# Kernel tuning notes

Hardware: AMD Instinct MI355X
Metric: run time of the kernel (lower is better)

The kernel has to match this reference:

```python
import jax, jax.numpy as jnp
import numpy as np

N_NODES = 30000
N_EDGES = 480000
NEG_SLOPE = 0.2  # PyG GATConv default negative_slope


def setup_inputs() -> dict:
    key = jax.random.key(0)
    ks = jax.random.split(key, 10)

    def glorot(k, shape, fan):
        return jax.random.normal(k, shape, jnp.float32) * (1.0 / np.sqrt(fan))

    x = jax.random.normal(ks[0], (N_NODES, 1024), jnp.float32)
    edge_index = jax.random.randint(ks[1], (2, N_EDGES), 0, N_NODES)
    # layer 1: in=1024 -> heads=8, C=64, concat -> 512
    W1 = glorot(ks[2], (1024, 512), 1024)
    a1_src = glorot(ks[3], (8, 64), 64)
    a1_dst = glorot(ks[4], (8, 64), 64)
    b1 = jnp.zeros((512,), jnp.float32)
    # layer 2: in=512 -> heads=1, C=256, no concat
    W2 = glorot(ks[5], (512, 256), 512)
    a2_src = glorot(ks[6], (1, 256), 256)
    a2_dst = glorot(ks[7], (1, 256), 256)
    b2 = jnp.zeros((256,), jnp.float32)
    return {"x": x, "edge_index": edge_index, "W1": W1, "a1_src": a1_src,
            "a1_dst": a1_dst, "b1": b1, "W2": W2, "a2_src": a2_src,
            "a2_dst": a2_dst, "b2": b2}


def gat_conv(x, src, dst, W, a_src, a_dst, bias, heads, channels, concat):
    """PyG-style GATConv (self-loops already included in src/dst)."""
    n = x.shape[0]
    h = (x @ W).reshape(n, heads, channels)          # [N, H, C]
    al_s = jnp.einsum('nhc,hc->nh', h, a_src)        # per-node src logits
    al_d = jnp.einsum('nhc,hc->nh', h, a_dst)        # per-node dst logits
    e = jax.nn.leaky_relu(al_s[src] + al_d[dst], NEG_SLOPE)   # [E, H]
    # segment softmax over edges grouped by destination node
    m = jax.ops.segment_max(e, dst, num_segments=n)
    p = jnp.exp(e - m[dst])
    s = jax.ops.segment_sum(p, dst, num_segments=n)
    alpha = p / s[dst]                               # [E, H]
    out = jax.ops.segment_sum(alpha[:, :, None] * h[src], dst, num_segments=n)
    out = out.reshape(n, heads * channels) if concat else out.mean(axis=1)
    return out + bias


def reference(x, edge_index, W1, a1_src, a1_dst, b1, W2, a2_src, a2_dst, b2):
    n = x.shape[0]
    loops = jnp.arange(n, dtype=edge_index.dtype)
    src = jnp.concatenate([edge_index[0], loops])    # add self-loops (PyG default)
    dst = jnp.concatenate([edge_index[1], loops])
    # eval mode: dropout is identity
    h = jax.nn.elu(gat_conv(x, src, dst, W1, a1_src, a1_dst, b1, 8, 64, True))
    out = gat_conv(h, src, dst, W2, a2_src, a2_dst, b2, 1, 256, False)
    return out
```

## Files before the change

### kernel.cpp

```cpp
#include <hip/hip_runtime.h>
#include <hip/hip_bf16.h>

typedef unsigned int uint;
typedef unsigned short ushort;
typedef __attribute__((ext_vector_type(8))) short short8;
typedef __attribute__((ext_vector_type(4))) short short4v;
typedef __attribute__((ext_vector_type(4))) float f32x4;

#define LEAKY 0.2f

__device__ __forceinline__ ushort f2bf(float f) {
  __hip_bfloat16 h = __float2bfloat16(f);
  return __builtin_bit_cast(ushort, h);
}
__device__ __forceinline__ float bf2f(ushort u) {
  uint v = ((uint)u) << 16;
  return __builtin_bit_cast(float, v);
}
__device__ __forceinline__ void gload_lds16(const void* g, void* l) {
  __builtin_amdgcn_global_load_lds(
      (const __attribute__((address_space(1))) void*)g,
      (__attribute__((address_space(3))) void*)l, 16, 0, 0);
}

__global__ void convw(const float* __restrict__ W, ushort* __restrict__ Wt,
                      int K, int N) {
  int idx = blockIdx.x * 256 + threadIdx.x;
  if (idx >= K * N) return;
  int nrow = idx / K;
  int k = idx - nrow * K;
  Wt[idx] = f2bf(W[(size_t)k * N + nrow]);
}

__global__ void zero2(int* a, int* b, int n) {
  int i = blockIdx.x * 256 + threadIdx.x;
  if (i < n) { a[i] = 0; b[i] = 0; }
}

__global__ void hist(const int* __restrict__ dst, int E, int n, int* cnt) {
  int e = blockIdx.x * 256 + threadIdx.x;
  if (e >= E + n) return;
  int d = (e < E) ? dst[e] : (e - E);
  atomicAdd(&cnt[d], 1);
}

__global__ __launch_bounds__(1024) void scan_fast(const int* __restrict__ cnt,
                                                  int* __restrict__ rp, int n) {
  __shared__ int wsum[16];
  __shared__ int woff[16];
  const int t = threadIdx.x;
  const int per = (n + 1023) / 1024;
  const int base = t * per;
  int local[32];
  int s = 0;
#pragma unroll
  for (int i = 0; i < 32; i++) {
    if (i >= per) break;
    int idx = base + i;
    int v = (idx < n) ? cnt[idx] : 0;
    local[i] = s;
    s += v;
  }
  const int lane = t & 63, wave = t >> 6;
  int incl = s;
#pragma unroll
  for (int off = 1; off < 64; off <<= 1) {
    int v = __shfl_up(incl, off);
    if (lane >= off) incl += v;
  }
  if (lane == 63) wsum[wave] = incl;
  __syncthreads();
  if (wave == 0 && lane < 16) {
    int v = wsum[lane];
    int wi = v;
#pragma unroll
    for (int off = 1; off < 16; off <<= 1) {
      int u = __shfl_up(wi, off);
      if (lane >= off) wi += u;
    }
    woff[lane] = wi - v;
  }
  __syncthreads();
  const int gexcl = woff[wave] + (incl - s);
#pragma unroll
  for (int i = 0; i < 32; i++) {
    if (i >= per) break;
    int idx = base + i;
    if (idx < n) rp[idx] = gexcl + local[i];
  }
  if (t == 1023) rp[n] = woff[15] + incl;
}

__global__ void scatter(const int* __restrict__ src, const int* __restrict__ dst,
                        int E, int n, const int* __restrict__ rp,
                        int* fill, int* __restrict__ csr) {
  int e = blockIdx.x * 256 + threadIdx.x;
  if (e >= E + n) return;
  int s, d;
  if (e < E) { s = src[e]; d = dst[e]; } else { s = d = e - E; }
  int pos = rp[d] + atomicAdd(&fill[d], 1);
  csr[pos] = s;
}

template <int ABYTES>
__global__ __launch_bounds__(512) void gemm_wide(
    const void* __restrict__ Av, const ushort* __restrict__ Bt,
    ushort* __restrict__ C, int M, int K, int N) {
  constexpr int BM = 128, BN = 256, BK = 32;
  constexpr int SPRA = (BK * ABYTES) / 16;
  constexpr int A_ITER = (BM * SPRA) / 512;
  __shared__ __align__(16) char As[BM * BK * ABYTES];
  __shared__ __align__(16) char Bs[BN * BK * 2];
  const int tid = threadIdx.x;
  const int wave = tid >> 6, lane = tid & 63;
  const int g = lane >> 4, r16 = lane & 15;
  const int nby = N / BN;
  const int bx = (int)blockIdx.x / nby;
  const int by = (int)blockIdx.x - bx * nby;
  const int bm = bx * BM, bn = by * BN;
  const int wm = (wave >> 2) * 64, wn = (wave & 3) * 64;

  f32x4 acc[4][4] = {};
  const char* A = (const char*)Av;

  for (int k0 = 0; k0 < K; k0 += BK) {
#pragma unroll
    for (int i = 0; i < A_ITER; i++) {
      int slot = i * 512 + tid;
      int row = slot / SPRA;
      int cp = slot % SPRA;
      int key = (ABYTES == 4) ? (row & 7) : ((row >> 1) & 3);
      int cl = cp ^ key;
      int arow = bm + row;
      arow = arow < M ? arow : M - 1;
      const char* gp = A + ((size_t)arow * K + k0) * ABYTES + cl * 16;
      char* lp = As + (i * 512 + wave * 64) * 16;
      gload_lds16(gp, lp);
    }
#pragma unroll
    for (int i = 0; i < 2; i++) {
      int slot = i * 512 + tid;
      int row = slot >> 2;
      int cp = slot & 3;
      int cl = cp ^ ((row >> 1) & 3);
      const char* gp = (const char*)(Bt + (size_t)(bn + row) * K + k0 + cl * 8);
      char* lp = Bs + (i * 512 + wave * 64) * 16;
      gload_lds16(gp, lp);
    }
    asm volatile("s_waitcnt vmcnt(0)" ::: "memory");
    __syncthreads();

    short8 af[4], bfr[4];
#pragma unroll
    for (int mi = 0; mi < 4; mi++) {
      int row = wm + mi * 16 + r16;
      if constexpr (ABYTES == 4) {
        int key = row & 7;
        f32x4 lo = *(const f32x4*)(As + (row * 8 + ((2 * g) ^ key)) * 16);
        f32x4 hi = *(const f32x4*)(As + (row * 8 + ((2 * g + 1) ^ key)) * 16);
        short8 s;
#pragma unroll
        for (int q = 0; q < 4; q++) {
          s[q] = (short)f2bf(lo[q]);
          s[q + 4] = (short)f2bf(hi[q]);
        }
        af[mi] = s;
      } else {
        int key = (row >> 1) & 3;
        af[mi] = *(const short8*)(As + (row * 4 + (g ^ key)) * 16);
      }
    }
#pragma unroll
    for (int ni = 0; ni < 4; ni++) {
      int row = wn + ni * 16 + r16;
      int key = (row >> 1) & 3;
      bfr[ni] = *(const short8*)(Bs + (row * 4 + (g ^ key)) * 16);
    }
#pragma unroll
    for (int mi = 0; mi < 4; mi++)
#pragma unroll
      for (int ni = 0; ni < 4; ni++)
        acc[mi][ni] = __builtin_amdgcn_mfma_f32_16x16x32_bf16(
            af[mi], bfr[ni], acc[mi][ni], 0, 0, 0);
    __syncthreads();
  }

#pragma unroll
  for (int mi = 0; mi < 4; mi++) {
#pragma unroll
    for (int j = 0; j < 4; j++) {
      int row = bm + wm + mi * 16 + g * 4 + j;
      if (row < M) {
#pragma unroll
        for (int ni = 0; ni < 4; ni++) {
          int col = bn + wn + ni * 16 + r16;
          C[(size_t)row * N + col] = f2bf(acc[mi][ni][j]);
        }
      }
    }
  }
}

__global__ void logits1(const ushort* __restrict__ h1, const float* __restrict__ a_s,
                        const float* __restrict__ a_d, float* __restrict__ al_s,
                        float* __restrict__ al_d, int n) {
  int node = blockIdx.x * 4 + (threadIdx.x >> 6);
  if (node >= n) return;
  int lane = threadIdx.x & 63;
  int c0 = lane * 8;
  short8 hv = *(const short8*)&h1[(size_t)node * 512 + c0];
  float ps = 0.f, pd = 0.f;
#pragma unroll
  for (int j = 0; j < 8; j++) {
    float f = bf2f((ushort)hv[j]);
    ps += f * a_s[c0 + j];
    pd += f * a_d[c0 + j];
  }
#pragma unroll
  for (int m = 1; m < 8; m <<= 1) {
    ps += __shfl_xor(ps, m);
    pd += __shfl_xor(pd, m);
  }
  if ((lane & 7) == 0) {
    al_s[node * 8 + (lane >> 3)] = ps;
    al_d[node * 8 + (lane >> 3)] = pd;
  }
}

__global__ void logits2(const ushort* __restrict__ h2, const float* __restrict__ a_s,
                        const float* __restrict__ a_d, float* __restrict__ al_s,
                        float* __restrict__ al_d, int n) {
  int node = blockIdx.x * 4 + (threadIdx.x >> 6);
  if (node >= n) return;
  int lane = threadIdx.x & 63;
  int c0 = lane * 4;
  short4v hv = *(const short4v*)&h2[(size_t)node * 256 + c0];
  float ps = 0.f, pd = 0.f;
#pragma unroll
  for (int j = 0; j < 4; j++) {
    float f = bf2f((ushort)hv[j]);
    ps += f * a_s[c0 + j];
    pd += f * a_d[c0 + j];
  }
#pragma unroll
  for (int m = 1; m < 64; m <<= 1) {
    ps += __shfl_xor(ps, m);
    pd += __shfl_xor(pd, m);
  }
  if (lane == 0) {
    al_s[node] = ps;
    al_d[node] = pd;
  }
}

__global__ void agg1(const int* __restrict__ rp, const int* __restrict__ csr,
                     const ushort* __restrict__ h1, const float* __restrict__ al_s,
                     const float* __restrict__ al_d, const float* __restrict__ b1,
                     ushort* __restrict__ h2in, int n) {
  int node = blockIdx.x * 4 + (threadIdx.x >> 6);
  if (node >= n) return;
  int lane = threadIdx.x & 63;
  int head = lane >> 3, c0 = lane * 8;
  float ad = al_d[node * 8 + head];
  int beg = rp[node], end = rp[node + 1];
  float sum = 0.f;
  float acc[8] = {};
  int j = beg;
  for (; j + 4 <= end; j += 4) {
    int s0 = csr[j], s1 = csr[j + 1], s2 = csr[j + 2], s3 = csr[j + 3];
    float e0 = al_s[s0 * 8 + head] + ad;
    float e1 = al_s[s1 * 8 + head] + ad;
    float e2 = al_s[s2 * 8 + head] + ad;
    float e3 = al_s[s3 * 8 + head] + ad;
    short8 v0 = *(const short8*)&h1[(size_t)s0 * 512 + c0];
    short8 v1 = *(const short8*)&h1[(size_t)s1 * 512 + c0];
    short8 v2 = *(const short8*)&h1[(size_t)s2 * 512 + c0];
    short8 v3 = *(const short8*)&h1[(size_t)s3 * 512 + c0];
    e0 = e0 > 0.f ? e0 : LEAKY * e0;
    e1 = e1 > 0.f ? e1 : LEAKY * e1;
    e2 = e2 > 0.f ? e2 : LEAKY * e2;
    e3 = e3 > 0.f ? e3 : LEAKY * e3;
    float p0 = __expf(e0), p1 = __expf(e1), p2 = __expf(e2), p3 = __expf(e3);
    sum += (p0 + p1) + (p2 + p3);
#pragma unroll
    for (int q = 0; q < 8; q++)
      acc[q] += p0 * bf2f((ushort)v0[q]) + p1 * bf2f((ushort)v1[q]) +
                p2 * bf2f((ushort)v2[q]) + p3 * bf2f((ushort)v3[q]);
  }
  for (; j < end; j++) {
    int s = csr[j];
    float e = al_s[s * 8 + head] + ad;
    e = e > 0.f ? e : LEAKY * e;
    float p = __expf(e);
    sum += p;
    short8 hv = *(const short8*)&h1[(size_t)s * 512 + c0];
#pragma unroll
    for (int q = 0; q < 8; q++) acc[q] += p * bf2f((ushort)hv[q]);
  }
  float inv = 1.0f / sum;
  short8 o;
#pragma unroll
  for (int q = 0; q < 8; q++) {
    float r = acc[q] * inv + b1[c0 + q];
    r = r > 0.f ? r : (__expf(r) - 1.0f);
    o[q] = (short)f2bf(r);
  }
  *(short8*)&h2in[(size_t)node * 512 + c0] = o;
}

__global__ void agg2(const int* __restrict__ rp, const int* __restrict__ csr,
                     const ushort* __restrict__ h2, const float* __restrict__ al_s,
                     const float* __restrict__ al_d, const float* __restrict__ b2,
                     float* __restrict__ out, int n) {
  int node = blockIdx.x * 4 + (threadIdx.x >> 6);
  if (node >= n) return;
  int lane = threadIdx.x & 63;
  int c0 = lane * 4;
  float ad = al_d[node];
  int beg = rp[node], end = rp[node + 1];
  float sum = 0.f;
  float a0 = 0.f, a1 = 0.f, a2 = 0.f, a3 = 0.f;
  int j = beg;
  for (; j + 4 <= end; j += 4) {
    int s0 = csr[j], s1 = csr[j + 1], s2 = csr[j + 2], s3 = csr[j + 3];
    float e0 = al_s[s0] + ad;
    float e1 = al_s[s1] + ad;
    float e2 = al_s[s2] + ad;
    float e3 = al_s[s3] + ad;
    short4v v0 = *(const short4v*)&h2[(size_t)s0 * 256 + c0];
    short4v v1 = *(const short4v*)&h2[(size_t)s1 * 256 + c0];
    short4v v2 = *(const short4v*)&h2[(size_t)s2 * 256 + c0];
    short4v v3 = *(const short4v*)&h2[(size_t)s3 * 256 + c0];
    e0 = e0 > 0.f ? e0 : LEAKY * e0;
    e1 = e1 > 0.f ? e1 : LEAKY * e1;
    e2 = e2 > 0.f ? e2 : LEAKY * e2;
    e3 = e3 > 0.f ? e3 : LEAKY * e3;
    float p0 = __expf(e0), p1 = __expf(e1), p2 = __expf(e2), p3 = __expf(e3);
    sum += (p0 + p1) + (p2 + p3);
    a0 += p0 * bf2f((ushort)v0[0]) + p1 * bf2f((ushort)v1[0]) +
          p2 * bf2f((ushort)v2[0]) + p3 * bf2f((ushort)v3[0]);
    a1 += p0 * bf2f((ushort)v0[1]) + p1 * bf2f((ushort)v1[1]) +
          p2 * bf2f((ushort)v2[1]) + p3 * bf2f((ushort)v3[1]);
    a2 += p0 * bf2f((ushort)v0[2]) + p1 * bf2f((ushort)v1[2]) +
          p2 * bf2f((ushort)v2[2]) + p3 * bf2f((ushort)v3[2]);
    a3 += p0 * bf2f((ushort)v0[3]) + p1 * bf2f((ushort)v1[3]) +
          p2 * bf2f((ushort)v2[3]) + p3 * bf2f((ushort)v3[3]);
  }
  for (; j < end; j++) {
    int s = csr[j];
    float e = al_s[s] + ad;
    e = e > 0.f ? e : LEAKY * e;
    float p = __expf(e);
    sum += p;
    short4v hv = *(const short4v*)&h2[(size_t)s * 256 + c0];
    a0 += p * bf2f((ushort)hv[0]);
    a1 += p * bf2f((ushort)hv[1]);
    a2 += p * bf2f((ushort)hv[2]);
    a3 += p * bf2f((ushort)hv[3]);
  }
  float inv = 1.0f / sum;
  f32x4 o;
  o[0] = a0 * inv + b2[c0 + 0];
  o[1] = a1 * inv + b2[c0 + 1];
  o[2] = a2 * inv + b2[c0 + 2];
  o[3] = a3 * inv + b2[c0 + 3];
  *(f32x4*)&out[(size_t)node * 256 + c0] = o;
}

extern "C" void kernel_launch(void* const* d_in, const int* in_sizes, int n_in,
                              void* d_out, int out_size, void* d_ws, size_t ws_size,
                              hipStream_t stream) {
  const float* x = (const float*)d_in[0];
  const int* ei = (const int*)d_in[1];
  const float* W1 = (const float*)d_in[2];
  const float* a1s = (const float*)d_in[3];
  const float* a1d = (const float*)d_in[4];
  const float* b1 = (const float*)d_in[5];
  const float* W2 = (const float*)d_in[6];
  const float* a2s = (const float*)d_in[7];
  const float* a2d = (const float*)d_in[8];
  const float* b2 = (const float*)d_in[9];
  float* out = (float*)d_out;

  const int n = in_sizes[0] / 1024;
  const int E = in_sizes[1] / 2;
  const int K1 = 1024, C1 = 512, C2 = 256;

  char* ws = (char*)d_ws;
  ushort* h1 = (ushort*)(ws + 0);
  ushort* h2in = (ushort*)(ws + 31000000);
  ushort* h2 = (ushort*)(ws + 62000000);
  float* al_s = (float*)(ws + 78000000);
  float* al_d = (float*)(ws + 79000000);
  float* al2s = (float*)(ws + 80000000);
  float* al2d = (float*)(ws + 80200000);
  ushort* W1t = (ushort*)(ws + 80400000);
  ushort* W2t = (ushort*)(ws + 81600000);
  int* cnt = (int*)(ws + 82000000);
  int* rp = (int*)(ws + 82200000);
  int* fill = (int*)(ws + 82400000);
  int* csr = (int*)(ws + 82600000);

  const int* esrc = ei;
  const int* edst = ei + E;
  const int ET = E + n;

  convw<<<(C1 * K1 + 255) / 256, 256, 0, stream>>>(W1, W1t, K1, C1);
  convw<<<(C2 * C1 + 255) / 256, 256, 0, stream>>>(W2, W2t, C1, C2);
  zero2<<<(n + 255) / 256, 256, 0, stream>>>(cnt, fill, n);
  hist<<<(ET + 255) / 256, 256, 0, stream>>>(edst, E, n, cnt);
  scan_fast<<<1, 1024, 0, stream>>>(cnt, rp, n);
  scatter<<<(ET + 255) / 256, 256, 0, stream>>>(esrc, edst, E, n, rp, fill, csr);

  const int gx1 = ((n + 127) / 128) * (C1 / 256);
  gemm_wide<4><<<gx1, 512, 0, stream>>>(x, W1t, h1, n, K1, C1);
  logits1<<<(n + 3) / 4, 256, 0, stream>>>(h1, a1s, a1d, al_s, al_d, n);
  agg1<<<(n + 3) / 4, 256, 0, stream>>>(rp, csr, h1, al_s, al_d, b1, h2in, n);

  const int gx2 = ((n + 127) / 128) * (C2 / 256);
  gemm_wide<2><<<gx2, 512, 0, stream>>>(h2in, W2t, h2, n, C1, C2);
  logits2<<<(n + 3) / 4, 256, 0, stream>>>(h2, a2s, a2d, al2s, al2d, n);
  agg2<<<(n + 3) / 4, 256, 0, stream>>>(rp, csr, h2, al2s, al2d, b2, out, n);
}
```

Before: 281.4 us.

## Double-buffer LDS in GEMM and remap workgroups across XCDs

The wide GEMM now keeps two LDS stages: it issues the global-to-LDS loads for the next K tile before computing on the current one, and uses partial vmcnt waits so the loads overlap with the MFMA work. Block IDs are also remapped so consecutive logical tiles land on the same XCD, meant to improve L2 reuse of the shared A/B tiles. This doubles LDS use per block, which may cut occupancy, and relies on hand-counted vmcnt values being correct. The renames in the aggregation kernels only avoid shadowing the new q/r variables.

```diff
diff --git a/kernel.cpp b/kernel.cpp
--- a/kernel.cpp
+++ b/kernel.cpp
@@ -109,21 +109,27 @@
   constexpr int BM = 128, BN = 256, BK = 32;
   constexpr int SPRA = (BK * ABYTES) / 16;
   constexpr int A_ITER = (BM * SPRA) / 512;
-  __shared__ __align__(16) char As[BM * BK * ABYTES];
-  __shared__ __align__(16) char Bs[BN * BK * 2];
+  __shared__ __align__(16) char As[2][BM * BK * ABYTES];
+  __shared__ __align__(16) char Bs[2][BN * BK * 2];
   const int tid = threadIdx.x;
   const int wave = tid >> 6, lane = tid & 63;
   const int g = lane >> 4, r16 = lane & 15;
+
+  const int nwg = (int)gridDim.x;
+  const int q = nwg >> 3, r = nwg & 7;
+  const int xcd = (int)blockIdx.x & 7, pos = (int)blockIdx.x >> 3;
+  const int wgid = (xcd < r ? xcd * (q + 1) : r * (q + 1) + (xcd - r) * q) + pos;
+
   const int nby = N / BN;
-  const int bx = (int)blockIdx.x / nby;
-  const int by = (int)blockIdx.x - bx * nby;
+  const int bx = wgid / nby;
+  const int by = wgid - bx * nby;
   const int bm = bx * BM, bn = by * BN;
   const int wm = (wave >> 2) * 64, wn = (wave & 3) * 64;
 
   f32x4 acc[4][4] = {};
   const char* A = (const char*)Av;
 
-  for (int k0 = 0; k0 < K; k0 += BK) {
+  auto stage = [&](int k0, int b) {
 #pragma unroll
     for (int i = 0; i < A_ITER; i++) {
       int slot = i * 512 + tid;
@@ -134,7 +140,7 @@
       int arow = bm + row;
       arow = arow < M ? arow : M - 1;
       const char* gp = A + ((size_t)arow * K + k0) * ABYTES + cl * 16;
-      char* lp = As + (i * 512 + wave * 64) * 16;
+      char* lp = &As[b][0] + (i * 512 + wave * 64) * 16;
       gload_lds16(gp, lp);
     }
 #pragma unroll
@@ -144,11 +150,26 @@
       int cp = slot & 3;
       int cl = cp ^ ((row >> 1) & 3);
       const char* gp = (const char*)(Bt + (size_t)(bn + row) * K + k0 + cl * 8);
-      char* lp = Bs + (i * 512 + wave * 64) * 16;
+      char* lp = &Bs[b][0] + (i * 512 + wave * 64) * 16;
       gload_lds16(gp, lp);
     }
-    asm volatile("s_waitcnt vmcnt(0)" ::: "memory");
-    __syncthreads();
+  };
+
+  const int nt = K / BK;
+  stage(0, 0);
+  int cur = 0;
+  for (int t = 0; t < nt; ++t) {
+    if (t + 1 < nt) {
+      stage((t + 1) * BK, cur ^ 1);
+      if constexpr (ABYTES == 4)
+        asm volatile("s_waitcnt vmcnt(4)" ::: "memory");
+      else
+        asm volatile("s_waitcnt vmcnt(3)" ::: "memory");
+    } else {
+      asm volatile("s_waitcnt vmcnt(0)" ::: "memory");
+    }
+    __builtin_amdgcn_sched_barrier(0);
+    __builtin_amdgcn_s_barrier();
 
     short8 af[4], bfr[4];
 #pragma unroll
@@ -156,25 +177,25 @@
       int row = wm + mi * 16 + r16;
       if constexpr (ABYTES == 4) {
         int key = row & 7;
-        f32x4 lo = *(const f32x4*)(As + (row * 8 + ((2 * g) ^ key)) * 16);
-        f32x4 hi = *(const f32x4*)(As + (row * 8 + ((2 * g + 1) ^ key)) * 16);
+        f32x4 lo = *(const f32x4*)(&As[cur][0] + (row * 8 + ((2 * g) ^ key)) * 16);
+        f32x4 hi = *(const f32x4*)(&As[cur][0] + (row * 8 + ((2 * g + 1) ^ key)) * 16);
         short8 s;
 #pragma unroll
-        for (int q = 0; q < 4; q++) {
-          s[q] = (short)f2bf(lo[q]);
-          s[q + 4] = (short)f2bf(hi[q]);
+        for (int qq = 0; qq < 4; qq++) {
+          s[qq] = (short)f2bf(lo[qq]);
+          s[qq + 4] = (short)f2bf(hi[qq]);
         }
         af[mi] = s;
       } else {
         int key = (row >> 1) & 3;
-        af[mi] = *(const short8*)(As + (row * 4 + (g ^ key)) * 16);
+        af[mi] = *(const short8*)(&As[cur][0] + (row * 4 + (g ^ key)) * 16);
       }
     }
 #pragma unroll
     for (int ni = 0; ni < 4; ni++) {
       int row = wn + ni * 16 + r16;
       int key = (row >> 1) & 3;
-      bfr[ni] = *(const short8*)(Bs + (row * 4 + (g ^ key)) * 16);
+      bfr[ni] = *(const short8*)(&Bs[cur][0] + (row * 4 + (g ^ key)) * 16);
     }
 #pragma unroll
     for (int mi = 0; mi < 4; mi++)
@@ -182,7 +203,8 @@
       for (int ni = 0; ni < 4; ni++)
         acc[mi][ni] = __builtin_amdgcn_mfma_f32_16x16x32_bf16(
             af[mi], bfr[ni], acc[mi][ni], 0, 0, 0);
-    __syncthreads();
+    __builtin_amdgcn_s_barrier();
+    cur ^= 1;
   }
 
 #pragma unroll
@@ -283,9 +305,9 @@
     float p0 = __expf(e0), p1 = __expf(e1), p2 = __expf(e2), p3 = __expf(e3);
     sum += (p0 + p1) + (p2 + p3);
 #pragma unroll
-    for (int q = 0; q < 8; q++)
-      acc[q] += p0 * bf2f((ushort)v0[q]) + p1 * bf2f((ushort)v1[q]) +
-                p2 * bf2f((ushort)v2[q]) + p3 * bf2f((ushort)v3[q]);
+    for (int qq = 0; qq < 8; qq++)
+      acc[qq] += p0 * bf2f((ushort)v0[qq]) + p1 * bf2f((ushort)v1[qq]) +
+                 p2 * bf2f((ushort)v2[qq]) + p3 * bf2f((ushort)v3[qq]);
   }
   for (; j < end; j++) {
     int s = csr[j];
@@ -295,15 +317,15 @@
     sum += p;
     short8 hv = *(const short8*)&h1[(size_t)s * 512 + c0];
 #pragma unroll
-    for (int q = 0; q < 8; q++) acc[q] += p * bf2f((ushort)hv[q]);
+    for (int qq = 0; qq < 8; qq++) acc[qq] += p * bf2f((ushort)hv[qq]);
   }
   float inv = 1.0f / sum;
   short8 o;
 #pragma unroll
-  for (int q = 0; q < 8; q++) {
-    float r = acc[q] * inv + b1[c0 + q];
-    r = r > 0.f ? r : (__expf(r) - 1.0f);
-    o[q] = (short)f2bf(r);
+  for (int qq = 0; qq < 8; qq++) {
+    float rr = acc[qq] * inv + b1[c0 + qq];
+    rr = rr > 0.f ? rr : (__expf(rr) - 1.0f);
+    o[qq] = (short)f2bf(rr);
   }
   *(short8*)&h2in[(size_t)node * 512 + c0] = o;
 }
```

Result: no change. 282.3 us (+0.3%).
